# Kernel optimization log

Measured on AMD Instinct MI355X. Metric: run time of the kernel, lower is better.

## Reference

```python
import jax, jax.numpy as jnp
import numpy as np

N_NODES = 200000
MAX_DEG = 128
S1, S2 = 25, 10  # neighbor sample sizes per hop (GraphSAGE defaults)


def setup_inputs() -> dict:
    key = jax.random.key(0)
    ks = jax.random.split(key, 9)
    F, H, C, B = 256, 128, 41, 1024
    return {
        "node_ids": jax.random.randint(ks[0], (B,), 0, N_NODES, dtype=jnp.int32),
        "features": jax.random.normal(ks[1], (N_NODES, F), dtype=jnp.float32),
        "adj_info": jax.random.randint(ks[2], (N_NODES, MAX_DEG), 0, N_NODES, dtype=jnp.int32),
        "W_self1": jax.random.normal(ks[3], (F, H), dtype=jnp.float32) * 0.05,
        "W_neigh1": jax.random.normal(ks[4], (F, H), dtype=jnp.float32) * 0.05,
        "W_self2": jax.random.normal(ks[5], (2 * H, H), dtype=jnp.float32) * 0.05,
        "W_neigh2": jax.random.normal(ks[6], (2 * H, H), dtype=jnp.float32) * 0.05,
        "W_pred": jax.random.normal(ks[7], (2 * H, C), dtype=jnp.float32) * 0.05,
        "b_pred": jnp.zeros((C,), dtype=jnp.float32),
    }


def _sample(adj_info, node_ids):
    """Uniform neighbor sampling: hop1 [B,S1], hop2 [B,S1,S2]."""
    k1, k2 = jax.random.split(jax.random.key(42))
    B = node_ids.shape[0]
    cols1 = jax.random.randint(k1, (B, S1), 0, MAX_DEG)
    hop1 = jnp.take_along_axis(adj_info[node_ids], cols1, axis=1)  # [B,S1]
    cols2 = jax.random.randint(k2, (B * S1, S2), 0, MAX_DEG)
    hop2 = jnp.take_along_axis(adj_info[hop1.reshape(-1)], cols2, axis=1)
    return hop1, hop2.reshape(B, S1, S2)


def _mean_agg(self_f, neigh_f, Ws, Wn, act):
    # GraphSAGE MeanAggregator with concat: [self@Ws ; mean(neigh)@Wn]
    neigh = neigh_f.mean(axis=-2)
    return act(jnp.concatenate([self_f @ Ws, neigh @ Wn], axis=-1))


def reference(node_ids, features, adj_info, W_self1, W_neigh1, W_self2, W_neigh2, W_pred, b_pred):
    hop1, hop2 = _sample(adj_info, node_ids)
    f0 = features[node_ids]      # [B,F]
    f1 = features[hop1]          # [B,S1,F]
    f2 = features[hop2]          # [B,S1,S2,F]

    h0 = _mean_agg(f0, f1, W_self1, W_neigh1, jax.nn.relu)   # [B,2H]
    h1 = _mean_agg(f1, f2, W_self1, W_neigh1, jax.nn.relu)   # [B,S1,2H]
    h = _mean_agg(h0, h1, W_self2, W_neigh2, lambda x: x)    # [B,2H]

    # tf.math.l2_normalize(x, 1): x * rsqrt(max(sum(x^2), 1e-12))
    h = h * jax.lax.rsqrt(jnp.maximum(jnp.sum(h * h, axis=1, keepdims=True), 1e-12))
    logits = h @ W_pred + b_pred
    return jax.nn.softmax(logits, axis=-1)
```

## Files before the change

kernel.cpp:

```cpp
#include <hip/hip_runtime.h>
#include <cstdint>
#include <cstddef>

#define BATCH 1024
#define S1 25
#define S2 10
#define FDIM 256
#define HDIM 128
#define NCLS 41
#define MAXDEG 128

typedef __attribute__((ext_vector_type(8))) short bf16x8;
typedef __attribute__((ext_vector_type(4))) float f32x4;

__host__ __device__ static inline void tf2x32(uint32_t k0, uint32_t k1,
                                              uint32_t c0, uint32_t c1,
                                              uint32_t& o0, uint32_t& o1) {
  const uint32_t ks2 = k0 ^ k1 ^ 0x1BD11BDAu;
  uint32_t x0 = c0 + k0, x1 = c1 + k1;
#define TFR(r) { x0 += x1; x1 = (x1 << (r)) | (x1 >> (32 - (r))); x1 ^= x0; }
  TFR(13) TFR(15) TFR(26) TFR(6)
  x0 += k1;  x1 += ks2 + 1u;
  TFR(17) TFR(29) TFR(16) TFR(24)
  x0 += ks2; x1 += k0 + 2u;
  TFR(13) TFR(15) TFR(26) TFR(6)
  x0 += k0;  x1 += k1 + 3u;
  TFR(17) TFR(29) TFR(16) TFR(24)
  x0 += k1;  x1 += ks2 + 4u;
  TFR(13) TFR(15) TFR(26) TFR(6)
  x0 += ks2; x1 += k0 + 5u;
#undef TFR
  o0 = x0; o1 = x1;
}

__device__ static inline uint32_t rand_bits_at(uint32_t kb0, uint32_t kb1, uint32_t j) {
  uint32_t o0, o1;
  tf2x32(kb0, kb1, 0u, j, o0, o1);
  return o0 ^ o1;
}

__device__ static inline ushort f2bf(float x) {
  uint32_t u = __float_as_uint(x);
  return (ushort)((u + 0x7fffu + ((u >> 16) & 1u)) >> 16);
}
__device__ static inline float bf2f(ushort u) {
  uint32_t v = ((uint32_t)u) << 16;
  return __uint_as_float(v);
}

__global__ void hop1_kernel(const int* __restrict__ node_ids,
                            const int* __restrict__ adj,
                            int* __restrict__ hop1,
                            uint32_t kb0, uint32_t kb1) {
  int j = blockIdx.x * blockDim.x + threadIdx.x;
  if (j >= BATCH * S1) return;
  uint32_t col = rand_bits_at(kb0, kb1, (uint32_t)j) & (MAXDEG - 1);
  int b = j / S1;
  hop1[j] = adj[(size_t)node_ids[b] * MAXDEG + col];
}

__global__ void hop2_kernel(const int* __restrict__ hop1,
                            const int* __restrict__ adj,
                            int* __restrict__ hop2,
                            uint32_t kb0, uint32_t kb1) {
  int j = blockIdx.x * blockDim.x + threadIdx.x;
  if (j >= BATCH * S1 * S2) return;
  uint32_t col = rand_bits_at(kb0, kb1, (uint32_t)j) & (MAXDEG - 1);
  hop2[j] = adj[(size_t)hop1[j / S2] * MAXDEG + col];
}

__global__ __launch_bounds__(256)
void prep_w_kernel(const float* __restrict__ Ws1, const float* __restrict__ Wn1,
                   ushort* __restrict__ WbT) {
  int h = blockIdx.x >> 7;
  int n = blockIdx.x & 127;
  int k = threadIdx.x;
  const float* W = h ? Wn1 : Ws1;
  WbT[((size_t)(h * HDIM + n)) * FDIM + k] = f2bf(W[(size_t)k * HDIM + n]);
}

__global__ __launch_bounds__(256)
void mean2_kernel(const float* __restrict__ feat, const int* __restrict__ hop2,
                  ushort* __restrict__ n2m) {
  int g = blockIdx.x * 4 + (threadIdx.x >> 6);
  int t = threadIdx.x & 63;
  const int* rowids = hop2 + (size_t)g * S2;
  float4 acc = make_float4(0.f, 0.f, 0.f, 0.f);
  for (int r = 0; r < S2; ++r) {
    float4 v = ((const float4*)(feat + (size_t)rowids[r] * FDIM))[t];
    acc.x += v.x; acc.y += v.y; acc.z += v.z; acc.w += v.w;
  }
  const float inv = 1.f / S2;
  ushort4 o;
  o.x = f2bf(acc.x * inv); o.y = f2bf(acc.y * inv);
  o.z = f2bf(acc.z * inv); o.w = f2bf(acc.w * inv);
  *(ushort4*)(n2m + (size_t)g * FDIM + t * 4) = o;
}

__global__ __launch_bounds__(256)
void gather_f1_kernel(const float* __restrict__ feat, const int* __restrict__ hop1,
                      ushort* __restrict__ f1b) {
  int g = blockIdx.x * 4 + (threadIdx.x >> 6);
  int t = threadIdx.x & 63;
  float4 v = ((const float4*)(feat + (size_t)hop1[g] * FDIM))[t];
  ushort4 o;
  o.x = f2bf(v.x); o.y = f2bf(v.y); o.z = f2bf(v.z); o.w = f2bf(v.w);
  *(ushort4*)(f1b + (size_t)g * FDIM + t * 4) = o;
}

__global__ __launch_bounds__(64)
void mean1_kernel(const ushort* __restrict__ f1b, float* __restrict__ n1m) {
  int b = blockIdx.x;
  int t = threadIdx.x;
  float4 acc = make_float4(0.f, 0.f, 0.f, 0.f);
  for (int r = 0; r < S1; ++r) {
    ushort4 v = *(const ushort4*)(f1b + (size_t)(b * S1 + r) * FDIM + t * 4);
    acc.x += bf2f(v.x); acc.y += bf2f(v.y); acc.z += bf2f(v.z); acc.w += bf2f(v.w);
  }
  const float inv = 1.f / S1;
  acc.x *= inv; acc.y *= inv; acc.z *= inv; acc.w *= inv;
  ((float4*)(n1m + (size_t)b * FDIM))[t] = acc;
}

__global__ __launch_bounds__(256, 2)
void mfma_h1_kernel(const ushort* __restrict__ f1b, const ushort* __restrict__ n2m,
                    const ushort* __restrict__ WbT, float* __restrict__ h1m) {
  const int half = blockIdx.y;
  const ushort* Amat = half ? n2m : f1b;
  const ushort* Bmat = WbT + (size_t)half * HDIM * FDIM;
  const int m0 = blockIdx.x * 64;
  const int tid = threadIdx.x;
  const int wave = tid >> 6;
  const int lane = tid & 63;
  const int lq = lane >> 4;
  const int lr = lane & 15;

  __shared__ ushort As[64][40];
  __shared__ ushort Bs[128][40];
  __shared__ float  Cs[64][132];

  f32x4 acc[4][2];
#pragma unroll
  for (int rt = 0; rt < 4; ++rt)
#pragma unroll
    for (int ct = 0; ct < 2; ++ct) acc[rt][ct] = (f32x4)(0.f);

  for (int k0 = 0; k0 < FDIM; k0 += 32) {
    {
      int row = tid >> 2, kc = (tid & 3) * 8;
      int4 v = *(const int4*)(Amat + (size_t)(m0 + row) * FDIM + k0 + kc);
      *(int4*)&As[row][kc] = v;
    }
#pragma unroll
    for (int i = 0; i < 2; ++i) {
      int idx = tid + i * 256;
      int n = idx >> 2, kc = (idx & 3) * 8;
      int4 v = *(const int4*)(Bmat + (size_t)n * FDIM + k0 + kc);
      *(int4*)&Bs[n][kc] = v;
    }
    __syncthreads();

    bf16x8 af[4];
#pragma unroll
    for (int rt = 0; rt < 4; ++rt)
      af[rt] = *(const bf16x8*)&As[rt * 16 + lr][lq * 8];
#pragma unroll
    for (int ct = 0; ct < 2; ++ct) {
      bf16x8 bf = *(const bf16x8*)&Bs[wave * 32 + ct * 16 + lr][lq * 8];
#pragma unroll
      for (int rt = 0; rt < 4; ++rt)
        acc[rt][ct] = __builtin_amdgcn_mfma_f32_16x16x32_bf16(af[rt], bf, acc[rt][ct], 0, 0, 0);
    }
    __syncthreads();
  }

#pragma unroll
  for (int rt = 0; rt < 4; ++rt)
#pragma unroll
    for (int ct = 0; ct < 2; ++ct)
#pragma unroll
      for (int r = 0; r < 4; ++r)
        Cs[rt * 16 + lq * 4 + r][wave * 32 + ct * 16 + lr] = fmaxf(acc[rt][ct][r], 0.f);
  __syncthreads();

  if (tid < 128) {
    const int c = tid;
    const int coff = half * HDIM + c;
    float s = 0.f;
    int curb = m0 / S1;
    for (int m = 0; m < 64; ++m) {
      int b = (m0 + m) / S1;
      if (b != curb) {
        atomicAdd(&h1m[(size_t)curb * (2 * HDIM) + coff], s * (1.f / S1));
        s = 0.f; curb = b;
      }
      s += Cs[m][c];
    }
    atomicAdd(&h1m[(size_t)curb * (2 * HDIM) + coff], s * (1.f / S1));
  }
}

template<int BM, int TM>
__global__ __launch_bounds__(256)
void gemm2_kernel(const float* __restrict__ A0, const int* __restrict__ idx0,
                  const float* __restrict__ A1, const int* __restrict__ idx1,
                  const float* __restrict__ gbase,
                  const float* __restrict__ W0, const float* __restrict__ W1,
                  float* __restrict__ Cout, int relu) {
  const int half = blockIdx.y;
  const float* A  = half ? A1 : A0;
  const int* idx  = half ? idx1 : idx0;
  const float* W  = half ? W1 : W0;
  const int coff  = half * HDIM;

  const int m0 = blockIdx.x * BM;
  const int tid = threadIdx.x;
  const int tx = tid & 31;
  const int ty = tid >> 5;

  __shared__ float As[32][BM];
  __shared__ float Bs[32][HDIM];

  float4 acc[TM];
#pragma unroll
  for (int r = 0; r < TM; ++r) acc[r] = make_float4(0.f, 0.f, 0.f, 0.f);

  for (int kt = 0; kt < FDIM / 32; ++kt) {
    const int k0 = kt * 32;
    constexpr int NF4 = BM * 8;
#pragma unroll
    for (int i = 0; i < (NF4 + 255) / 256; ++i) {
      int f4 = tid + i * 256;
      if (f4 < NF4) {
        int row = f4 >> 3;
        int kc  = (f4 & 7) << 2;
        const float* rp = idx ? (gbase + (size_t)idx[m0 + row] * FDIM)
                              : (A + (size_t)(m0 + row) * FDIM);
        float4 v = *(const float4*)(rp + k0 + kc);
        As[kc + 0][row] = v.x;
        As[kc + 1][row] = v.y;
        As[kc + 2][row] = v.z;
        As[kc + 3][row] = v.w;
      }
    }
#pragma unroll
    for (int i = 0; i < 4; ++i) {
      int f4 = tid + i * 256;
      int kr = f4 >> 5;
      int c4 = (f4 & 31) << 2;
      *(float4*)&Bs[kr][c4] = *(const float4*)(W + (size_t)(k0 + kr) * HDIM + c4);
    }
    __syncthreads();
#pragma unroll
    for (int kk = 0; kk < 32; ++kk) {
      float a[TM];
#pragma unroll
      for (int r = 0; r < TM; ++r) a[r] = As[kk][ty * TM + r];
      float4 b = *(const float4*)&Bs[kk][tx << 2];
#pragma unroll
      for (int r = 0; r < TM; ++r) {
        acc[r].x += a[r] * b.x; acc[r].y += a[r] * b.y;
        acc[r].z += a[r] * b.z; acc[r].w += a[r] * b.w;
      }
    }
    __syncthreads();
  }
#pragma unroll
  for (int r = 0; r < TM; ++r) {
    int m = m0 + ty * TM + r;
    float4 v = acc[r];
    if (relu) {
      v.x = fmaxf(v.x, 0.f); v.y = fmaxf(v.y, 0.f);
      v.z = fmaxf(v.z, 0.f); v.w = fmaxf(v.w, 0.f);
    }
    *(float4*)(Cout + (size_t)m * (2 * HDIM) + coff + (tx << 2)) = v;
  }
}

__global__ __launch_bounds__(64)
void head_kernel(const float* __restrict__ hmat,
                 const float* __restrict__ Wp,
                 const float* __restrict__ bp,
                 float* __restrict__ out) {
  const int b = blockIdx.x;
  const int t = threadIdx.x;
  __shared__ float hl[2 * HDIM];
  float4 hv = ((const float4*)(hmat + (size_t)b * 2 * HDIM))[t];
  float ss = hv.x * hv.x + hv.y * hv.y + hv.z * hv.z + hv.w * hv.w;
#pragma unroll
  for (int off = 32; off; off >>= 1) ss += __shfl_xor(ss, off, 64);
  float s = rsqrtf(fmaxf(ss, 1e-12f));
  float4 hn = make_float4(hv.x * s, hv.y * s, hv.z * s, hv.w * s);
  ((float4*)hl)[t] = hn;
  __syncthreads();
  float logit = -1e30f;
  if (t < NCLS) {
    logit = bp[t];
    for (int k = 0; k < 2 * HDIM; ++k) logit += hl[k] * Wp[k * NCLS + t];
  }
  float mx = logit;
#pragma unroll
  for (int off = 32; off; off >>= 1) mx = fmaxf(mx, __shfl_xor(mx, off, 64));
  float e = (t < NCLS) ? expf(logit - mx) : 0.f;
  float sum = e;
#pragma unroll
  for (int off = 32; off; off >>= 1) sum += __shfl_xor(sum, off, 64);
  if (t < NCLS) out[(size_t)b * NCLS + t] = e / sum;
}

extern "C" void kernel_launch(void* const* d_in, const int* in_sizes, int n_in,
                              void* d_out, int out_size, void* d_ws, size_t ws_size,
                              hipStream_t stream) {
  const int*   node_ids = (const int*)d_in[0];
  const float* features = (const float*)d_in[1];
  const int*   adj      = (const int*)d_in[2];
  const float* Ws1      = (const float*)d_in[3];
  const float* Wn1      = (const float*)d_in[4];
  const float* Ws2      = (const float*)d_in[5];
  const float* Wn2      = (const float*)d_in[6];
  const float* Wp       = (const float*)d_in[7];
  const float* bp       = (const float*)d_in[8];
  float* out = (float*)d_out;

  char* ws = (char*)d_ws;
  int*    hop1 = (int*)(ws + 0);
  int*    hop2 = (int*)(ws + 102400);
  ushort* f1b  = (ushort*)(ws + 1126400);
  ushort* n2m  = (ushort*)(ws + 14233600);
  ushort* WbT  = (ushort*)(ws + 27340800);
  float*  n1m  = (float*)(ws + 27471872);
  float*  h1m  = (float*)(ws + 28520448);
  float*  h0   = (float*)(ws + 29569024);
  float*  hh   = (float*)(ws + 30617600);

  uint32_t k1_0, k1_1, k2_0, k2_1, kb1_0, kb1_1, kb2_0, kb2_1;
  tf2x32(0u, 42u, 0u, 0u, k1_0, k1_1);
  tf2x32(0u, 42u, 0u, 1u, k2_0, k2_1);
  tf2x32(k1_0, k1_1, 0u, 1u, kb1_0, kb1_1);
  tf2x32(k2_0, k2_1, 0u, 1u, kb2_0, kb2_1);

  hop1_kernel<<<(BATCH * S1 + 255) / 256, 256, 0, stream>>>(node_ids, adj, hop1, kb1_0, kb1_1);
  hop2_kernel<<<(BATCH * S1 * S2 + 255) / 256, 256, 0, stream>>>(hop1, adj, hop2, kb2_0, kb2_1);

  prep_w_kernel<<<256, 256, 0, stream>>>(Ws1, Wn1, WbT);
  hipMemsetAsync(h1m, 0, (size_t)BATCH * 2 * HDIM * sizeof(float), stream);

  gather_f1_kernel<<<BATCH * S1 / 4, 256, 0, stream>>>(features, hop1, f1b);
  mean2_kernel<<<BATCH * S1 / 4, 256, 0, stream>>>(features, hop2, n2m);
  mean1_kernel<<<BATCH, 64, 0, stream>>>(f1b, n1m);

  dim3 gBig(BATCH * S1 / 64, 2);
  mfma_h1_kernel<<<gBig, 256, 0, stream>>>(f1b, n2m, WbT, h1m);

  dim3 gSmall(BATCH / 16, 2);
  gemm2_kernel<16, 2><<<gSmall, 256, 0, stream>>>(nullptr, node_ids, n1m, nullptr,
                                                  features, Ws1, Wn1, h0, 1);
  gemm2_kernel<16, 2><<<gSmall, 256, 0, stream>>>(h0, nullptr, h1m, nullptr,
                                                  features, Ws2, Wn2, hh, 0);
  head_kernel<<<BATCH, 64, 0, stream>>>(hh, Wp, bp, out);
}
```

Baseline: 410.4 us.

## Fuse sampling, gathers and means into one prep kernel; fuse tail GEMMs with head

Sampling of hop1 and hop2, the hop2 mean, the hop1 mean, the weight transpose and the h1m zeroing are merged into a single multi-role prep kernel. Hop2 indices now live in registers and reach lanes through wave shuffles. The MFMA kernel gathers and converts f1 rows directly from features instead of reading a materialized bf16 f1 buffer. The two small GEMMs, the L2 normalize and the softmax head are fused into one tail kernel that handles four rows per block. This removes several launches and intermediate round trips to global memory, in exchange for some redundant feature gathers (the hop1 rows are read in both prep and MFMA) and a less parallel tail GEMM.

```diff
diff --git a/kernel.cpp b/kernel.cpp
--- a/kernel.cpp
+++ b/kernel.cpp
@@ -43,90 +43,79 @@
   uint32_t u = __float_as_uint(x);
   return (ushort)((u + 0x7fffu + ((u >> 16) & 1u)) >> 16);
 }
-__device__ static inline float bf2f(ushort u) {
-  uint32_t v = ((uint32_t)u) << 16;
-  return __uint_as_float(v);
-}
-
-__global__ void hop1_kernel(const int* __restrict__ node_ids,
-                            const int* __restrict__ adj,
-                            int* __restrict__ hop1,
-                            uint32_t kb0, uint32_t kb1) {
-  int j = blockIdx.x * blockDim.x + threadIdx.x;
-  if (j >= BATCH * S1) return;
-  uint32_t col = rand_bits_at(kb0, kb1, (uint32_t)j) & (MAXDEG - 1);
-  int b = j / S1;
-  hop1[j] = adj[(size_t)node_ids[b] * MAXDEG + col];
-}
-
-__global__ void hop2_kernel(const int* __restrict__ hop1,
-                            const int* __restrict__ adj,
-                            int* __restrict__ hop2,
-                            uint32_t kb0, uint32_t kb1) {
-  int j = blockIdx.x * blockDim.x + threadIdx.x;
-  if (j >= BATCH * S1 * S2) return;
-  uint32_t col = rand_bits_at(kb0, kb1, (uint32_t)j) & (MAXDEG - 1);
-  hop2[j] = adj[(size_t)hop1[j / S2] * MAXDEG + col];
-}
 
 __global__ __launch_bounds__(256)
-void prep_w_kernel(const float* __restrict__ Ws1, const float* __restrict__ Wn1,
-                   ushort* __restrict__ WbT) {
-  int h = blockIdx.x >> 7;
-  int n = blockIdx.x & 127;
-  int k = threadIdx.x;
-  const float* W = h ? Wn1 : Ws1;
-  WbT[((size_t)(h * HDIM + n)) * FDIM + k] = f2bf(W[(size_t)k * HDIM + n]);
-}
-
-__global__ __launch_bounds__(256)
-void mean2_kernel(const float* __restrict__ feat, const int* __restrict__ hop2,
-                  ushort* __restrict__ n2m) {
-  int g = blockIdx.x * 4 + (threadIdx.x >> 6);
-  int t = threadIdx.x & 63;
-  const int* rowids = hop2 + (size_t)g * S2;
-  float4 acc = make_float4(0.f, 0.f, 0.f, 0.f);
-  for (int r = 0; r < S2; ++r) {
-    float4 v = ((const float4*)(feat + (size_t)rowids[r] * FDIM))[t];
-    acc.x += v.x; acc.y += v.y; acc.z += v.z; acc.w += v.w;
-  }
-  const float inv = 1.f / S2;
-  ushort4 o;
-  o.x = f2bf(acc.x * inv); o.y = f2bf(acc.y * inv);
-  o.z = f2bf(acc.z * inv); o.w = f2bf(acc.w * inv);
-  *(ushort4*)(n2m + (size_t)g * FDIM + t * 4) = o;
-}
-
-__global__ __launch_bounds__(256)
-void gather_f1_kernel(const float* __restrict__ feat, const int* __restrict__ hop1,
-                      ushort* __restrict__ f1b) {
-  int g = blockIdx.x * 4 + (threadIdx.x >> 6);
-  int t = threadIdx.x & 63;
-  float4 v = ((const float4*)(feat + (size_t)hop1[g] * FDIM))[t];
-  ushort4 o;
-  o.x = f2bf(v.x); o.y = f2bf(v.y); o.z = f2bf(v.z); o.w = f2bf(v.w);
-  *(ushort4*)(f1b + (size_t)g * FDIM + t * 4) = o;
-}
-
-__global__ __launch_bounds__(64)
-void mean1_kernel(const ushort* __restrict__ f1b, float* __restrict__ n1m) {
-  int b = blockIdx.x;
-  int t = threadIdx.x;
-  float4 acc = make_float4(0.f, 0.f, 0.f, 0.f);
-  for (int r = 0; r < S1; ++r) {
-    ushort4 v = *(const ushort4*)(f1b + (size_t)(b * S1 + r) * FDIM + t * 4);
-    acc.x += bf2f(v.x); acc.y += bf2f(v.y); acc.z += bf2f(v.z); acc.w += bf2f(v.w);
-  }
-  const float inv = 1.f / S1;
-  acc.x *= inv; acc.y *= inv; acc.z *= inv; acc.w *= inv;
-  ((float4*)(n1m + (size_t)b * FDIM))[t] = acc;
+void prep_kernel(const int* __restrict__ node_ids, const float* __restrict__ feat,
+                 const int* __restrict__ adj,
+                 const float* __restrict__ Ws1, const float* __restrict__ Wn1,
+                 int* __restrict__ hop1g, ushort* __restrict__ n2m,
+                 float* __restrict__ n1m, ushort* __restrict__ WbT,
+                 float* __restrict__ h1m,
+                 uint32_t kb1_0, uint32_t kb1_1, uint32_t kb2_0, uint32_t kb2_1) {
+  const int blk = blockIdx.x;
+  const int t = threadIdx.x;
+  if (blk < 6400) {
+    const int wave = t >> 6, lane = t & 63;
+    const int g = blk * 4 + wave;
+    const int b = g / S1;
+    int hop1v = 0;
+    if (lane == 0) {
+      uint32_t c1 = rand_bits_at(kb1_0, kb1_1, (uint32_t)g) & (MAXDEG - 1);
+      hop1v = adj[(size_t)node_ids[b] * MAXDEG + c1];
+    }
+    hop1v = __shfl(hop1v, 0, 64);
+    if (lane == 0) hop1g[g] = hop1v;
+    int r2id = 0;
+    if (lane < S2) {
+      uint32_t c2 = rand_bits_at(kb2_0, kb2_1, (uint32_t)(g * S2 + lane)) & (MAXDEG - 1);
+      r2id = adj[(size_t)hop1v * MAXDEG + c2];
+    }
+    float4 acc = make_float4(0.f, 0.f, 0.f, 0.f);
+#pragma unroll
+    for (int r = 0; r < S2; ++r) {
+      int rid = __shfl(r2id, r, 64);
+      float4 v = ((const float4*)(feat + (size_t)rid * FDIM))[lane];
+      acc.x += v.x; acc.y += v.y; acc.z += v.z; acc.w += v.w;
+    }
+    const float inv = 1.f / S2;
+    ushort4 o;
+    o.x = f2bf(acc.x * inv); o.y = f2bf(acc.y * inv);
+    o.z = f2bf(acc.z * inv); o.w = f2bf(acc.w * inv);
+    *(ushort4*)(n2m + (size_t)g * FDIM + lane * 4) = o;
+  } else if (blk < 6656) {
+    const int wave = t >> 6, lane = t & 63;
+    const int b = (blk - 6400) * 4 + wave;
+    int h1v = 0;
+    if (lane < S1) {
+      uint32_t c1 = rand_bits_at(kb1_0, kb1_1, (uint32_t)(b * S1 + lane)) & (MAXDEG - 1);
+      h1v = adj[(size_t)node_ids[b] * MAXDEG + c1];
+    }
+    float4 acc = make_float4(0.f, 0.f, 0.f, 0.f);
+#pragma unroll
+    for (int r = 0; r < S1; ++r) {
+      int rid = __shfl(h1v, r, 64);
+      float4 v = ((const float4*)(feat + (size_t)rid * FDIM))[lane];
+      acc.x += v.x; acc.y += v.y; acc.z += v.z; acc.w += v.w;
+    }
+    const float inv = 1.f / S1;
+    acc.x *= inv; acc.y *= inv; acc.z *= inv; acc.w *= inv;
+    ((float4*)(n1m + (size_t)b * FDIM))[lane] = acc;
+  } else if (blk < 6912) {
+    const int idx = blk - 6656;
+    const int h = idx >> 7, n = idx & 127;
+    const float* W = h ? Wn1 : Ws1;
+    WbT[(size_t)idx * FDIM + t] = f2bf(W[(size_t)t * HDIM + n]);
+  } else {
+    const int i = (blk - 6912) * 256 + t;
+    ((float4*)h1m)[i] = make_float4(0.f, 0.f, 0.f, 0.f);
+  }
 }
 
 __global__ __launch_bounds__(256, 2)
-void mfma_h1_kernel(const ushort* __restrict__ f1b, const ushort* __restrict__ n2m,
-                    const ushort* __restrict__ WbT, float* __restrict__ h1m) {
+void mfma_h1_kernel(const int* __restrict__ hop1g, const float* __restrict__ feat,
+                    const ushort* __restrict__ n2m, const ushort* __restrict__ WbT,
+                    float* __restrict__ h1m) {
   const int half = blockIdx.y;
-  const ushort* Amat = half ? n2m : f1b;
   const ushort* Bmat = WbT + (size_t)half * HDIM * FDIM;
   const int m0 = blockIdx.x * 64;
   const int tid = threadIdx.x;
@@ -138,6 +127,10 @@
   __shared__ ushort As[64][40];
   __shared__ ushort Bs[128][40];
   __shared__ float  Cs[64][132];
+  __shared__ int rowid[64];
+
+  if (half == 0 && tid < 64) rowid[tid] = hop1g[m0 + tid];
+  __syncthreads();
 
   f32x4 acc[4][2];
 #pragma unroll
@@ -146,17 +139,25 @@
     for (int ct = 0; ct < 2; ++ct) acc[rt][ct] = (f32x4)(0.f);
 
   for (int k0 = 0; k0 < FDIM; k0 += 32) {
-    {
-      int row = tid >> 2, kc = (tid & 3) * 8;
-      int4 v = *(const int4*)(Amat + (size_t)(m0 + row) * FDIM + k0 + kc);
+    const int row = tid >> 2, kc = (tid & 3) * 8;
+    if (half == 0) {
+      const float* rp = feat + (size_t)rowid[row] * FDIM + k0 + kc;
+      float4 v0 = *(const float4*)rp;
+      float4 v1 = *(const float4*)(rp + 4);
+      union { ushort u[8]; int4 v; } pk;
+      pk.u[0] = f2bf(v0.x); pk.u[1] = f2bf(v0.y); pk.u[2] = f2bf(v0.z); pk.u[3] = f2bf(v0.w);
+      pk.u[4] = f2bf(v1.x); pk.u[5] = f2bf(v1.y); pk.u[6] = f2bf(v1.z); pk.u[7] = f2bf(v1.w);
+      *(int4*)&As[row][kc] = pk.v;
+    } else {
+      int4 v = *(const int4*)(n2m + (size_t)(m0 + row) * FDIM + k0 + kc);
       *(int4*)&As[row][kc] = v;
     }
 #pragma unroll
     for (int i = 0; i < 2; ++i) {
       int idx = tid + i * 256;
-      int n = idx >> 2, kc = (idx & 3) * 8;
-      int4 v = *(const int4*)(Bmat + (size_t)n * FDIM + k0 + kc);
-      *(int4*)&Bs[n][kc] = v;
+      int n = idx >> 2, kc2 = (idx & 3) * 8;
+      int4 v = *(const int4*)(Bmat + (size_t)n * FDIM + k0 + kc2);
+      *(int4*)&Bs[n][kc2] = v;
     }
     __syncthreads();
 
@@ -200,112 +201,120 @@
   }
 }
 
-template<int BM, int TM>
 __global__ __launch_bounds__(256)
-void gemm2_kernel(const float* __restrict__ A0, const int* __restrict__ idx0,
-                  const float* __restrict__ A1, const int* __restrict__ idx1,
-                  const float* __restrict__ gbase,
-                  const float* __restrict__ W0, const float* __restrict__ W1,
-                  float* __restrict__ Cout, int relu) {
-  const int half = blockIdx.y;
-  const float* A  = half ? A1 : A0;
-  const int* idx  = half ? idx1 : idx0;
-  const float* W  = half ? W1 : W0;
-  const int coff  = half * HDIM;
-
-  const int m0 = blockIdx.x * BM;
-  const int tid = threadIdx.x;
-  const int tx = tid & 31;
-  const int ty = tid >> 5;
-
-  __shared__ float As[32][BM];
-  __shared__ float Bs[32][HDIM];
-
-  float4 acc[TM];
-#pragma unroll
-  for (int r = 0; r < TM; ++r) acc[r] = make_float4(0.f, 0.f, 0.f, 0.f);
-
-  for (int kt = 0; kt < FDIM / 32; ++kt) {
-    const int k0 = kt * 32;
-    constexpr int NF4 = BM * 8;
-#pragma unroll
-    for (int i = 0; i < (NF4 + 255) / 256; ++i) {
-      int f4 = tid + i * 256;
-      if (f4 < NF4) {
-        int row = f4 >> 3;
-        int kc  = (f4 & 7) << 2;
-        const float* rp = idx ? (gbase + (size_t)idx[m0 + row] * FDIM)
-                              : (A + (size_t)(m0 + row) * FDIM);
-        float4 v = *(const float4*)(rp + k0 + kc);
-        As[kc + 0][row] = v.x;
-        As[kc + 1][row] = v.y;
-        As[kc + 2][row] = v.z;
-        As[kc + 3][row] = v.w;
+void tail_kernel(const int* __restrict__ node_ids, const float* __restrict__ feat,
+                 const float* __restrict__ n1m, const float* __restrict__ h1m,
+                 const float* __restrict__ Ws1, const float* __restrict__ Wn1,
+                 const float* __restrict__ Ws2, const float* __restrict__ Wn2,
+                 const float* __restrict__ Wp, const float* __restrict__ bp,
+                 float* __restrict__ out) {
+  const int b0 = blockIdx.x * 4;
+  const int t = threadIdx.x;
+  const int wave = t >> 6, lane = t & 63;
+
+  __shared__ float A0[4][256];
+  __shared__ float A1[4][256];
+  __shared__ float H1[4][256];
+  __shared__ float H0[4][256];
+  __shared__ float HN[4][256];
+  __shared__ float red[4][4];
+  __shared__ float scl[4];
+  __shared__ float lg[4][NCLS];
+  __shared__ float sm[4][2];
+
+  {
+    const int r = wave;
+    const int nid = node_ids[b0 + r];
+    ((float4*)A0[r])[lane] = ((const float4*)(feat + (size_t)nid * FDIM))[lane];
+    ((float4*)A1[r])[lane] = ((const float4*)(n1m + (size_t)(b0 + r) * FDIM))[lane];
+    ((float4*)H1[r])[lane] = ((const float4*)(h1m + (size_t)(b0 + r) * FDIM))[lane];
+  }
+  __syncthreads();
+
+  const int h = t >> 7, c = t & 127;
+  {
+    const float* W = h ? Wn1 : Ws1;
+    const float* Ap = h ? &A1[0][0] : &A0[0][0];
+    float acc[4] = {0.f, 0.f, 0.f, 0.f};
+    for (int k4 = 0; k4 < 64; ++k4) {
+      float w0 = W[(size_t)(k4 * 4 + 0) * HDIM + c];
+      float w1 = W[(size_t)(k4 * 4 + 1) * HDIM + c];
+      float w2 = W[(size_t)(k4 * 4 + 2) * HDIM + c];
+      float w3 = W[(size_t)(k4 * 4 + 3) * HDIM + c];
+#pragma unroll
+      for (int r = 0; r < 4; ++r) {
+        float4 a = ((const float4*)(Ap + r * 256))[k4];
+        acc[r] += a.x * w0 + a.y * w1 + a.z * w2 + a.w * w3;
       }
     }
 #pragma unroll
-    for (int i = 0; i < 4; ++i) {
-      int f4 = tid + i * 256;
-      int kr = f4 >> 5;
-      int c4 = (f4 & 31) << 2;
-      *(float4*)&Bs[kr][c4] = *(const float4*)(W + (size_t)(k0 + kr) * HDIM + c4);
-    }
-    __syncthreads();
-#pragma unroll
-    for (int kk = 0; kk < 32; ++kk) {
-      float a[TM];
-#pragma unroll
-      for (int r = 0; r < TM; ++r) a[r] = As[kk][ty * TM + r];
-      float4 b = *(const float4*)&Bs[kk][tx << 2];
-#pragma unroll
-      for (int r = 0; r < TM; ++r) {
-        acc[r].x += a[r] * b.x; acc[r].y += a[r] * b.y;
-        acc[r].z += a[r] * b.z; acc[r].w += a[r] * b.w;
+    for (int r = 0; r < 4; ++r) H0[r][t] = fmaxf(acc[r], 0.f);
+  }
+  __syncthreads();
+
+  float hv[4];
+  {
+    const float* W = h ? Wn2 : Ws2;
+    const float* Ap = h ? &H1[0][0] : &H0[0][0];
+    float acc[4] = {0.f, 0.f, 0.f, 0.f};
+    for (int k4 = 0; k4 < 64; ++k4) {
+      float w0 = W[(size_t)(k4 * 4 + 0) * HDIM + c];
+      float w1 = W[(size_t)(k4 * 4 + 1) * HDIM + c];
+      float w2 = W[(size_t)(k4 * 4 + 2) * HDIM + c];
+      float w3 = W[(size_t)(k4 * 4 + 3) * HDIM + c];
+#pragma unroll
+      for (int r = 0; r < 4; ++r) {
+        float4 a = ((const float4*)(Ap + r * 256))[k4];
+        acc[r] += a.x * w0 + a.y * w1 + a.z * w2 + a.w * w3;
       }
     }
-    __syncthreads();
-  }
-#pragma unroll
-  for (int r = 0; r < TM; ++r) {
-    int m = m0 + ty * TM + r;
-    float4 v = acc[r];
-    if (relu) {
-      v.x = fmaxf(v.x, 0.f); v.y = fmaxf(v.y, 0.f);
-      v.z = fmaxf(v.z, 0.f); v.w = fmaxf(v.w, 0.f);
-    }
-    *(float4*)(Cout + (size_t)m * (2 * HDIM) + coff + (tx << 2)) = v;
-  }
-}
-
-__global__ __launch_bounds__(64)
-void head_kernel(const float* __restrict__ hmat,
-                 const float* __restrict__ Wp,
-                 const float* __restrict__ bp,
-                 float* __restrict__ out) {
-  const int b = blockIdx.x;
-  const int t = threadIdx.x;
-  __shared__ float hl[2 * HDIM];
-  float4 hv = ((const float4*)(hmat + (size_t)b * 2 * HDIM))[t];
-  float ss = hv.x * hv.x + hv.y * hv.y + hv.z * hv.z + hv.w * hv.w;
-#pragma unroll
-  for (int off = 32; off; off >>= 1) ss += __shfl_xor(ss, off, 64);
-  float s = rsqrtf(fmaxf(ss, 1e-12f));
-  float4 hn = make_float4(hv.x * s, hv.y * s, hv.z * s, hv.w * s);
-  ((float4*)hl)[t] = hn;
-  __syncthreads();
-  float logit = -1e30f;
-  if (t < NCLS) {
-    logit = bp[t];
-    for (int k = 0; k < 2 * HDIM; ++k) logit += hl[k] * Wp[k * NCLS + t];
-  }
-  float mx = logit;
-#pragma unroll
-  for (int off = 32; off; off >>= 1) mx = fmaxf(mx, __shfl_xor(mx, off, 64));
-  float e = (t < NCLS) ? expf(logit - mx) : 0.f;
-  float sum = e;
-#pragma unroll
-  for (int off = 32; off; off >>= 1) sum += __shfl_xor(sum, off, 64);
-  if (t < NCLS) out[(size_t)b * NCLS + t] = e / sum;
+#pragma unroll
+    for (int r = 0; r < 4; ++r) hv[r] = acc[r];
+  }
+
+  {
+    float ss[4];
+#pragma unroll
+    for (int r = 0; r < 4; ++r) ss[r] = hv[r] * hv[r];
+#pragma unroll
+    for (int off = 32; off; off >>= 1)
+#pragma unroll
+      for (int r = 0; r < 4; ++r) ss[r] += __shfl_xor(ss[r], off, 64);
+    if (lane == 0) {
+#pragma unroll
+      for (int r = 0; r < 4; ++r) red[wave][r] = ss[r];
+    }
+  }
+  __syncthreads();
+  if (t < 4) {
+    float tot = red[0][t] + red[1][t] + red[2][t] + red[3][t];
+    scl[t] = rsqrtf(fmaxf(tot, 1e-12f));
+  }
+  __syncthreads();
+#pragma unroll
+  for (int r = 0; r < 4; ++r) HN[r][t] = hv[r] * scl[r];
+  __syncthreads();
+
+  int rr = 0, cc = 0;
+  float logit = 0.f;
+  if (t < 4 * NCLS) {
+    rr = t / NCLS; cc = t - rr * NCLS;
+    float acc = bp[cc];
+    for (int k = 0; k < 2 * HDIM; ++k) acc += HN[rr][k] * Wp[(size_t)k * NCLS + cc];
+    lg[rr][cc] = acc;
+    logit = acc;
+  }
+  __syncthreads();
+  if (t < 4) {
+    float m = -1e30f;
+    for (int i = 0; i < NCLS; ++i) m = fmaxf(m, lg[t][i]);
+    float s = 0.f;
+    for (int i = 0; i < NCLS; ++i) s += expf(lg[t][i] - m);
+    sm[t][0] = m; sm[t][1] = s;
+  }
+  __syncthreads();
+  if (t < 4 * NCLS)
+    out[(size_t)(b0 + rr) * NCLS + cc] = expf(logit - sm[rr][0]) / sm[rr][1];
 }
 
 extern "C" void kernel_launch(void* const* d_in, const int* in_sizes, int n_in,
@@ -324,14 +333,10 @@
 
   char* ws = (char*)d_ws;
   int*    hop1 = (int*)(ws + 0);
-  int*    hop2 = (int*)(ws + 102400);
-  ushort* f1b  = (ushort*)(ws + 1126400);
-  ushort* n2m  = (ushort*)(ws + 14233600);
-  ushort* WbT  = (ushort*)(ws + 27340800);
-  float*  n1m  = (float*)(ws + 27471872);
-  float*  h1m  = (float*)(ws + 28520448);
-  float*  h0   = (float*)(ws + 29569024);
-  float*  hh   = (float*)(ws + 30617600);
+  ushort* n2m  = (ushort*)(ws + 102400);
+  ushort* WbT  = (ushort*)(ws + 13209600);
+  float*  n1m  = (float*)(ws + 13340672);
+  float*  h1m  = (float*)(ws + 14389248);
 
   uint32_t k1_0, k1_1, k2_0, k2_1, kb1_0, kb1_1, kb2_0, kb2_1;
   tf2x32(0u, 42u, 0u, 0u, k1_0, k1_1);
@@ -339,23 +344,13 @@
   tf2x32(k1_0, k1_1, 0u, 1u, kb1_0, kb1_1);
   tf2x32(k2_0, k2_1, 0u, 1u, kb2_0, kb2_1);
 
-  hop1_kernel<<<(BATCH * S1 + 255) / 256, 256, 0, stream>>>(node_ids, adj, hop1, kb1_0, kb1_1);
-  hop2_kernel<<<(BATCH * S1 * S2 + 255) / 256, 256, 0, stream>>>(hop1, adj, hop2, kb2_0, kb2_1);
-
-  prep_w_kernel<<<256, 256, 0, stream>>>(Ws1, Wn1, WbT);
-  hipMemsetAsync(h1m, 0, (size_t)BATCH * 2 * HDIM * sizeof(float), stream);
-
-  gather_f1_kernel<<<BATCH * S1 / 4, 256, 0, stream>>>(features, hop1, f1b);
-  mean2_kernel<<<BATCH * S1 / 4, 256, 0, stream>>>(features, hop2, n2m);
-  mean1_kernel<<<BATCH, 64, 0, stream>>>(f1b, n1m);
+  prep_kernel<<<7168, 256, 0, stream>>>(node_ids, features, adj, Ws1, Wn1,
+                                        hop1, n2m, n1m, WbT, h1m,
+                                        kb1_0, kb1_1, kb2_0, kb2_1);
 
   dim3 gBig(BATCH * S1 / 64, 2);
-  mfma_h1_kernel<<<gBig, 256, 0, stream>>>(f1b, n2m, WbT, h1m);
-
-  dim3 gSmall(BATCH / 16, 2);
-  gemm2_kernel<16, 2><<<gSmall, 256, 0, stream>>>(nullptr, node_ids, n1m, nullptr,
-                                                  features, Ws1, Wn1, h0, 1);
-  gemm2_kernel<16, 2><<<gSmall, 256, 0, stream>>>(h0, nullptr, h1m, nullptr,
-                                                  features, Ws2, Wn2, hh, 0);
-  head_kernel<<<BATCH, 64, 0, stream>>>(hh, Wp, bp, out);
-}
+  mfma_h1_kernel<<<gBig, 256, 0, stream>>>(hop1, features, n2m, WbT, h1m);
+
+  tail_kernel<<<BATCH / 4, 256, 0, stream>>>(node_ids, features, n1m, h1m,
+                                             Ws1, Wn1, Ws2, Wn2, Wp, bp, out);
+}
```

Result: faster. 386.3 us (-5.9%).
